# Kernel tuning notes

Measured on AMD Instinct MI355X. Metric: run time of the kernel, lower is better.

The kernel has to match this reference:

```python
import jax, jax.numpy as jnp
import numpy as np

H = 24  # hidden size hard-coded in TrendGRU


def setup_inputs() -> dict:
    key = jax.random.key(0)
    ks = jax.random.split(key, 7)
    B, T = 32768, 512
    s_ih = 1.0 / np.sqrt(H)
    x = jax.random.normal(ks[0], (B, T, 1), dtype=jnp.float32)
    # GRUCell params (PyTorch layout: rows ordered r, z, n)
    W_ih = jax.random.uniform(ks[1], (3 * H, 1), minval=-s_ih, maxval=s_ih, dtype=jnp.float32)
    W_hh = jax.random.uniform(ks[2], (3 * H, H), minval=-s_ih, maxval=s_ih, dtype=jnp.float32)
    b_ih = jax.random.uniform(ks[3], (3 * H,), minval=-s_ih, maxval=s_ih, dtype=jnp.float32)
    b_hh = jax.random.uniform(ks[4], (3 * H,), minval=-s_ih, maxval=s_ih, dtype=jnp.float32)
    fc_w = jax.random.uniform(ks[5], (2, H), minval=-s_ih, maxval=s_ih, dtype=jnp.float32)
    fc_b = jax.random.uniform(ks[6], (2,), minval=-s_ih, maxval=s_ih, dtype=jnp.float32)
    return {"x": x, "W_ih": W_ih, "b_ih": b_ih, "W_hh": W_hh, "b_hh": b_hh,
            "fc_w": fc_w, "fc_b": fc_b}


def _gru_scan(x, W_ih, b_ih, W_hh, b_hh):
    B = x.shape[0]
    # precompute input projections for all timesteps: (B,T,1)@(1,3H) -> (T,B,3H)
    gx = jnp.einsum('bti,gi->tbg', x, W_ih) + b_ih
    h0 = jnp.zeros((B, H), dtype=x.dtype)

    def step(h, gx_t):
        gh = h @ W_hh.T + b_hh                      # (B, 3H)
        xr, xz, xn = jnp.split(gx_t, 3, axis=-1)    # PyTorch order r, z, n
        hr, hz, hn = jnp.split(gh, 3, axis=-1)
        r = jax.nn.sigmoid(xr + hr)
        z = jax.nn.sigmoid(xz + hz)
        n = jnp.tanh(xn + r * hn)
        h_new = (1.0 - z) * n + z * h
        return h_new, None

    h_final, _ = jax.lax.scan(step, h0, gx)
    return h_final


def reference(x, W_ih, b_ih, W_hh, b_hh, fc_w, fc_b):
    h = _gru_scan(x, W_ih, b_ih, W_hh, b_hh)
    return h @ fc_w.T + fc_b  # (B, 2)
```

## Files before the change

### kernel.cpp

```cpp
#include <hip/hip_runtime.h>


#define GRU_T 512
#define FS 28

typedef __attribute__((ext_vector_type(8)))  short bf16x8;
typedef __attribute__((ext_vector_type(16))) float f32x16;
typedef __attribute__((ext_vector_type(2)))  float f32x2;
typedef __attribute__((ext_vector_type(2)))  unsigned uint2v;

__device__ __forceinline__ float bf16hi_f(float v) {
    unsigned u = __float_as_uint(v);
    u = (u + 0x7FFFu + ((u >> 16) & 1u)) & 0xFFFF0000u;
    return __uint_as_float(u);
}
__device__ __forceinline__ unsigned bf16_rne(float v) {
    unsigned u = __float_as_uint(v);
    return (u + 0x7FFFu + ((u >> 16) & 1u)) >> 16;
}
__device__ __forceinline__ unsigned cvt_pk_bf16(float lo, float hi) {
    unsigned r;
    asm("v_cvt_pk_bf16_f32 %0, %1, %2" : "=v"(r) : "v"(lo), "v"(hi));
    return r;
}
__device__ __forceinline__ f32x16 mfma32(bf16x8 a, bf16x8 b, f32x16 c) {
    return __builtin_amdgcn_mfma_f32_32x32x16_bf16(a, b, c, 0, 0, 0);
}

__global__ __launch_bounds__(64) void trend_gru_mfma32(
    const float* __restrict__ x,
    const float* __restrict__ W_ih,
    const float* __restrict__ b_ih,
    const float* __restrict__ W_hh,
    const float* __restrict__ b_hh,
    const float* __restrict__ fc_w,
    const float* __restrict__ fc_b,
    float* __restrict__ out)
{
    const int lane = threadIdx.x;
    const int e    = lane & 31;
    const int half = lane >> 5;
    const int elem0 = blockIdx.x * 32;

    __shared__ __align__(16) float Flds[32 * FS];

    const float L2E = 1.4426950408889634f;

    bf16x8 A[3][2][2];
#pragma unroll
    for (int g = 0; g < 3; ++g) {
        const float sc = (g == 2) ? 2.0f * L2E : L2E;
        const int m = e;
        const bool valid = m < 24;
        const int R = g * 24 + (valid ? m : 0);
        const float wx = (g < 2 && valid) ? sc * W_ih[R] : 0.0f;
        const float bb = valid ? sc * ((g < 2) ? (b_ih[R] + b_hh[R]) : b_hh[R]) : 0.0f;
        const float wxh = bf16hi_f(wx), bbh = bf16hi_f(bb);
#pragma unroll
        for (int s = 0; s < 2; ++s) {
            bf16x8 fh, fl;
#pragma unroll
            for (int jj = 0; jj < 8; ++jj) {
                const int k = s * 16 + half * 8 + jj;
                float vh = 0.0f, vl = 0.0f;
                if (valid && k < 24) {
                    const float w  = sc * W_hh[R * 24 + k];
                    const float wh = bf16hi_f(w);
                    vh = wh; vl = w - wh;
                } else if (valid) {
                    if (k == 24 || k == 25)      vh = wxh;
                    else if (k == 26)            vh = wx - wxh;
                    else if (k == 27)            vh = bbh;
                    else if (k == 28)            vh = bb - bbh;
                }
                fh[jj] = (short)bf16_rne(vh);
                fl[jj] = (short)bf16_rne(vl);
            }
            A[g][s][0] = fh;
            A[g][s][1] = fl;
        }
    }

    f32x2 wn2[6], bn2[6];
#pragma unroll
    for (int p = 0; p < 6; ++p) {
#pragma unroll
        for (int c = 0; c < 2; ++c) {
            const int s = p * 2 + c;
            const int j = (s & 3) + 8 * (s >> 2) + 4 * half;
            wn2[p][c] = 2.0f * L2E * W_ih[48 + j];
            bn2[p][c] = 2.0f * L2E * b_ih[48 + j];
        }
    }

    const float* xp = x + (size_t)(elem0 + e) * GRU_T;
    float xv = xp[0];

    f32x2 h2[6];
#pragma unroll
    for (int p = 0; p < 6; ++p) { h2[p].x = 0.0f; h2[p].y = 0.0f; }

    f32x2 aX2[6];
#pragma unroll
    for (int p = 0; p < 6; ++p) {
        const f32x2 xb = {xv, xv};
        aX2[p] = __builtin_elementwise_fma(wn2[p], xb, bn2[p]);
    }

    unsigned P0 = 0, P1 = 0, P2 = 0, P3 = 0, P4 = 0, P5 = 0;

    const f32x16 z16 = {0.f,0.f,0.f,0.f,0.f,0.f,0.f,0.f,
                        0.f,0.f,0.f,0.f,0.f,0.f,0.f,0.f};

#pragma unroll 2
    for (int t = 0; t < GRU_T; ++t) {
        const uint2v r02 = __builtin_amdgcn_permlane32_swap(P0, P2, false, false);
        const uint2v r13 = __builtin_amdgcn_permlane32_swap(P1, P3, false, false);
        uint4 b0q;
        b0q.x = r02.x;
        b0q.y = r13.x;
        b0q.z = r02.y;
        b0q.w = r13.y;

        const uint2v r44 = __builtin_amdgcn_permlane32_swap(P4, P4, false, false);
        const uint2v r55 = __builtin_amdgcn_permlane32_swap(P5, P5, false, false);
        uint4 b1q;
        b1q.x = P4;
        b1q.y = P5;
        b1q.z = r44.y;
        b1q.w = r55.y;
        if (half) {
            const unsigned xy = cvt_pk_bf16(xv, 1.0f);
            const float    xh = __uint_as_float(xy << 16);
            const unsigned xx = cvt_pk_bf16(xv, xv - xh);
            b1q.x = xx;
            b1q.y = xy;
            b1q.z = 0x00003F80u;
            b1q.w = 0u;
        }
        const bf16x8 B0 = *(const bf16x8*)&b0q;
        const bf16x8 B1 = *(const bf16x8*)&b1q;
        const float xnext = xp[(t + 1 < GRU_T) ? t + 1 : t];

        f32x16 aR = mfma32(A[0][0][0], B0, z16);
        aR = mfma32(A[0][0][1], B0, aR);
        aR = mfma32(A[0][1][0], B1, aR);
        aR = mfma32(A[0][1][1], B1, aR);
        f32x16 aZ = mfma32(A[1][0][0], B0, z16);
        aZ = mfma32(A[1][0][1], B0, aZ);
        aZ = mfma32(A[1][1][0], B1, aZ);
        aZ = mfma32(A[1][1][1], B1, aZ);
        f32x16 aN = mfma32(A[2][0][0], B0, z16);
        aN = mfma32(A[2][0][1], B0, aN);
        aN = mfma32(A[2][1][0], B1, aN);
        aN = mfma32(A[2][1][1], B1, aN);

#pragma unroll
        for (int G = 0; G < 3; ++G) {
            unsigned pk[2];
#pragma unroll
            for (int p = 0; p < 2; ++p) {
                const int s = G * 4 + p * 2;
                f32x2 er2, ez2, qi2, ev2, rv2;
                er2.x = __builtin_amdgcn_exp2f(-aR[s]);
                er2.y = __builtin_amdgcn_exp2f(-aR[s + 1]);
                ez2.x = __builtin_amdgcn_exp2f(-aZ[s]);
                ez2.y = __builtin_amdgcn_exp2f(-aZ[s + 1]);
                const f32x2 one2 = {1.0f, 1.0f};
                const f32x2 dr2 = er2 + one2;
                const f32x2 dz2 = ez2 + one2;
                const f32x2 pp2 = dr2 * dz2;
                qi2.x = __builtin_amdgcn_rcpf(pp2.x);
                qi2.y = __builtin_amdgcn_rcpf(pp2.y);
                const f32x2 rr2 = qi2 * dz2;
                const f32x2 zz2 = qi2 * dr2;
                const f32x2 an2 = {aN[s], aN[s + 1]};
                const f32x2 u2  = __builtin_elementwise_fma(rr2, an2, aX2[G * 2 + p]);
                ev2.x = __builtin_amdgcn_exp2f(u2.x);
                ev2.y = __builtin_amdgcn_exp2f(u2.y);
                const f32x2 dv2 = ev2 + one2;
                rv2.x = __builtin_amdgcn_rcpf(dv2.x);
                rv2.y = __builtin_amdgcn_rcpf(dv2.y);
                const f32x2 m2   = {-2.0f, -2.0f};
                const f32x2 nn2  = __builtin_elementwise_fma(m2, rv2, one2);
                const f32x2 hm2  = h2[G * 2 + p] - nn2;
                const f32x2 hn2  = __builtin_elementwise_fma(zz2, hm2, nn2);
                h2[G * 2 + p] = hn2;
                pk[p] = cvt_pk_bf16(hn2.x, hn2.y);
            }
            if (G == 0)      { P0 = pk[0]; P1 = pk[1]; }
            else if (G == 1) { P2 = pk[0]; P3 = pk[1]; }
            else             { P4 = pk[0]; P5 = pk[1]; }
        }

        xv = xnext;
#pragma unroll
        for (int p = 0; p < 6; ++p) {
            const f32x2 xb = {xv, xv};
            aX2[p] = __builtin_elementwise_fma(wn2[p], xb, bn2[p]);
        }
    }

#pragma unroll
    for (int G = 0; G < 3; ++G) {
        float4 f4;
        f4.x = h2[G * 2 + 0].x; f4.y = h2[G * 2 + 0].y;
        f4.z = h2[G * 2 + 1].x; f4.w = h2[G * 2 + 1].y;
        *(float4*)(&Flds[e * FS + G * 8 + half * 4]) = f4;
    }
    if (lane < 32) {
        float o0 = fc_b[0], o1 = fc_b[1];
#pragma unroll
        for (int j = 0; j < 24; ++j) {
            const float hv = Flds[lane * FS + j];
            o0 = fmaf(hv, fc_w[j],      o0);
            o1 = fmaf(hv, fc_w[24 + j], o1);
        }
        float2 o; o.x = o0; o.y = o1;
        *(float2*)(out + (size_t)(elem0 + lane) * 2) = o;
    }
}

extern "C" void kernel_launch(void* const* d_in, const int* in_sizes, int n_in,
                              void* d_out, int out_size, void* d_ws, size_t ws_size,
                              hipStream_t stream) {
    const float* x    = (const float*)d_in[0];
    const float* W_ih = (const float*)d_in[1];
    const float* b_ih = (const float*)d_in[2];
    const float* W_hh = (const float*)d_in[3];
    const float* b_hh = (const float*)d_in[4];
    const float* fc_w = (const float*)d_in[5];
    const float* fc_b = (const float*)d_in[6];
    float* out = (float*)d_out;

    const int B = in_sizes[0] / GRU_T;
    const int grid = B / 32;
    trend_gru_mfma32<<<grid, 64, 0, stream>>>(x, W_ih, b_ih, W_hh, b_hh,
                                              fc_w, fc_b, out);
}
```

Measured before the change: 454.5 us.

## Software-pipeline GRU step so B1 MFMAs overlap remaining gate epilogue

Restructures the recurrence loop so that the hidden-state slice feeding the second MFMA operand (P4/P5 plus the x/bias terms) is computed first. Its MFMAs are issued while the epilogue for the other four pairs is still running, and accumulation order is reversed so the B0 MFMAs finish the accumulator. Each pair also shares a single reciprocal between two lanes' denominators for both the sigmoid and tanh paths, cutting transcendental ops. The aim is to hide MFMA latency on the serial critical path, at the cost of extra live accumulator registers, a peeled prologue/epilogue, and a slight precision change from the shared reciprocal.

```diff
diff --git a/kernel.cpp b/kernel.cpp
--- a/kernel.cpp
+++ b/kernel.cpp
@@ -25,6 +25,39 @@
 }
 __device__ __forceinline__ f32x16 mfma32(bf16x8 a, bf16x8 b, f32x16 c) {
     return __builtin_amdgcn_mfma_f32_32x32x16_bf16(a, b, c, 0, 0, 0);
+}
+
+__device__ __forceinline__ unsigned pair_epi(float ar0, float ar1,
+                                             float az0, float az1,
+                                             float an0, float an1,
+                                             const f32x2 aX, f32x2& h)
+{
+    const f32x2 one2 = {1.0f, 1.0f};
+    f32x2 er2, ez2, ev2;
+    er2.x = __builtin_amdgcn_exp2f(-ar0);
+    er2.y = __builtin_amdgcn_exp2f(-ar1);
+    ez2.x = __builtin_amdgcn_exp2f(-az0);
+    ez2.y = __builtin_amdgcn_exp2f(-az1);
+    const f32x2 dr2 = er2 + one2;
+    const f32x2 dz2 = ez2 + one2;
+    const f32x2 pp2 = dr2 * dz2;
+    const float  Q  = __builtin_amdgcn_rcpf(pp2.x * pp2.y);
+    f32x2 qi2; qi2.x = Q * pp2.y; qi2.y = Q * pp2.x;
+    const f32x2 rr2 = qi2 * dz2;
+    const f32x2 zz2 = qi2 * dr2;
+    const f32x2 an2 = {an0, an1};
+    const f32x2 u2  = __builtin_elementwise_fma(rr2, an2, aX);
+    ev2.x = __builtin_amdgcn_exp2f(u2.x);
+    ev2.y = __builtin_amdgcn_exp2f(u2.y);
+    const f32x2 dv2 = ev2 + one2;
+    const float  Qn = __builtin_amdgcn_rcpf(dv2.x * dv2.y);
+    f32x2 rv2; rv2.x = Qn * dv2.y; rv2.y = Qn * dv2.x;
+    const f32x2 m2  = {-2.0f, -2.0f};
+    const f32x2 nn2 = __builtin_elementwise_fma(m2, rv2, one2);
+    const f32x2 hm2 = h - nn2;
+    const f32x2 hn2 = __builtin_elementwise_fma(zz2, hm2, nn2);
+    h = hn2;
+    return cvt_pk_bf16(hn2.x, hn2.y);
 }
 
 __global__ __launch_bounds__(64) void trend_gru_mfma32(
@@ -94,11 +127,16 @@
     }
 
     const float* xp = x + (size_t)(elem0 + e) * GRU_T;
-    float xv = xp[0];
 
     f32x2 h2[6];
 #pragma unroll
     for (int p = 0; p < 6; ++p) { h2[p].x = 0.0f; h2[p].y = 0.0f; }
+
+    const f32x16 z16 = {0.f,0.f,0.f,0.f,0.f,0.f,0.f,0.f,
+                        0.f,0.f,0.f,0.f,0.f,0.f,0.f,0.f};
+
+    float xv    = xp[0];
+    float xnext = xp[1];
 
     f32x2 aX2[6];
 #pragma unroll
@@ -107,99 +145,88 @@
         aX2[p] = __builtin_elementwise_fma(wn2[p], xb, bn2[p]);
     }
 
-    unsigned P0 = 0, P1 = 0, P2 = 0, P3 = 0, P4 = 0, P5 = 0;
-
-    const f32x16 z16 = {0.f,0.f,0.f,0.f,0.f,0.f,0.f,0.f,
-                        0.f,0.f,0.f,0.f,0.f,0.f,0.f,0.f};
-
-#pragma unroll 2
-    for (int t = 0; t < GRU_T; ++t) {
-        const uint2v r02 = __builtin_amdgcn_permlane32_swap(P0, P2, false, false);
-        const uint2v r13 = __builtin_amdgcn_permlane32_swap(P1, P3, false, false);
+    f32x16 aR, aZ, aN;
+    {
+        uint4 b1q; b1q.x = 0u; b1q.y = 0u; b1q.z = 0u; b1q.w = 0u;
+        if (half) {
+            const unsigned xy = cvt_pk_bf16(xv, 1.0f);
+            const float    xh = __uint_as_float(xy << 16);
+            const unsigned xx = cvt_pk_bf16(xv, xv - xh);
+            b1q.x = xx; b1q.y = xy; b1q.z = 0x00003F80u; b1q.w = 0u;
+        }
+        const bf16x8 B1 = *(const bf16x8*)&b1q;
+        uint4 b0q; b0q.x = 0u; b0q.y = 0u; b0q.z = 0u; b0q.w = 0u;
+        const bf16x8 B0 = *(const bf16x8*)&b0q;
+        aR = mfma32(A[0][1][0], B1, mfma32(A[0][1][1], B1, z16));
+        aZ = mfma32(A[1][1][0], B1, mfma32(A[1][1][1], B1, z16));
+        aN = mfma32(A[2][1][0], B1, mfma32(A[2][1][1], B1, z16));
+        aR = mfma32(A[0][0][0], B0, mfma32(A[0][0][1], B0, aR));
+        aZ = mfma32(A[1][0][0], B0, mfma32(A[1][0][1], B0, aZ));
+        aN = mfma32(A[2][0][0], B0, mfma32(A[2][0][1], B0, aN));
+    }
+
+#pragma unroll 1
+    for (int t = 0; t < GRU_T - 1; ++t) {
+        const unsigned nP4 = pair_epi(aR[8],  aR[9],  aZ[8],  aZ[9],
+                                      aN[8],  aN[9],  aX2[4], h2[4]);
+        const unsigned nP5 = pair_epi(aR[10], aR[11], aZ[10], aZ[11],
+                                      aN[10], aN[11], aX2[5], h2[5]);
+        const uint2v r44 = __builtin_amdgcn_permlane32_swap(nP4, nP4, false, false);
+        const uint2v r55 = __builtin_amdgcn_permlane32_swap(nP5, nP5, false, false);
+        uint4 b1q;
+        b1q.x = nP4;
+        b1q.y = nP5;
+        b1q.z = r44.y;
+        b1q.w = r55.y;
+        if (half) {
+            const unsigned xy = cvt_pk_bf16(xnext, 1.0f);
+            const float    xh = __uint_as_float(xy << 16);
+            const unsigned xx = cvt_pk_bf16(xnext, xnext - xh);
+            b1q.x = xx; b1q.y = xy; b1q.z = 0x00003F80u; b1q.w = 0u;
+        }
+        const bf16x8 B1 = *(const bf16x8*)&b1q;
+
+        f32x16 nR = mfma32(A[0][1][0], B1, mfma32(A[0][1][1], B1, z16));
+        f32x16 nZ = mfma32(A[1][1][0], B1, mfma32(A[1][1][1], B1, z16));
+        f32x16 nN = mfma32(A[2][1][0], B1, mfma32(A[2][1][1], B1, z16));
+
+        const unsigned nP0 = pair_epi(aR[0], aR[1], aZ[0], aZ[1],
+                                      aN[0], aN[1], aX2[0], h2[0]);
+        const unsigned nP1 = pair_epi(aR[2], aR[3], aZ[2], aZ[3],
+                                      aN[2], aN[3], aX2[1], h2[1]);
+        const unsigned nP2 = pair_epi(aR[4], aR[5], aZ[4], aZ[5],
+                                      aN[4], aN[5], aX2[2], h2[2]);
+        const unsigned nP3 = pair_epi(aR[6], aR[7], aZ[6], aZ[7],
+                                      aN[6], aN[7], aX2[3], h2[3]);
+        const uint2v r02 = __builtin_amdgcn_permlane32_swap(nP0, nP2, false, false);
+        const uint2v r13 = __builtin_amdgcn_permlane32_swap(nP1, nP3, false, false);
         uint4 b0q;
         b0q.x = r02.x;
         b0q.y = r13.x;
         b0q.z = r02.y;
         b0q.w = r13.y;
-
-        const uint2v r44 = __builtin_amdgcn_permlane32_swap(P4, P4, false, false);
-        const uint2v r55 = __builtin_amdgcn_permlane32_swap(P5, P5, false, false);
-        uint4 b1q;
-        b1q.x = P4;
-        b1q.y = P5;
-        b1q.z = r44.y;
-        b1q.w = r55.y;
-        if (half) {
-            const unsigned xy = cvt_pk_bf16(xv, 1.0f);
-            const float    xh = __uint_as_float(xy << 16);
-            const unsigned xx = cvt_pk_bf16(xv, xv - xh);
-            b1q.x = xx;
-            b1q.y = xy;
-            b1q.z = 0x00003F80u;
-            b1q.w = 0u;
-        }
         const bf16x8 B0 = *(const bf16x8*)&b0q;
-        const bf16x8 B1 = *(const bf16x8*)&b1q;
-        const float xnext = xp[(t + 1 < GRU_T) ? t + 1 : t];
-
-        f32x16 aR = mfma32(A[0][0][0], B0, z16);
-        aR = mfma32(A[0][0][1], B0, aR);
-        aR = mfma32(A[0][1][0], B1, aR);
-        aR = mfma32(A[0][1][1], B1, aR);
-        f32x16 aZ = mfma32(A[1][0][0], B0, z16);
-        aZ = mfma32(A[1][0][1], B0, aZ);
-        aZ = mfma32(A[1][1][0], B1, aZ);
-        aZ = mfma32(A[1][1][1], B1, aZ);
-        f32x16 aN = mfma32(A[2][0][0], B0, z16);
-        aN = mfma32(A[2][0][1], B0, aN);
-        aN = mfma32(A[2][1][0], B1, aN);
-        aN = mfma32(A[2][1][1], B1, aN);
-
-#pragma unroll
-        for (int G = 0; G < 3; ++G) {
-            unsigned pk[2];
-#pragma unroll
-            for (int p = 0; p < 2; ++p) {
-                const int s = G * 4 + p * 2;
-                f32x2 er2, ez2, qi2, ev2, rv2;
-                er2.x = __builtin_amdgcn_exp2f(-aR[s]);
-                er2.y = __builtin_amdgcn_exp2f(-aR[s + 1]);
-                ez2.x = __builtin_amdgcn_exp2f(-aZ[s]);
-                ez2.y = __builtin_amdgcn_exp2f(-aZ[s + 1]);
-                const f32x2 one2 = {1.0f, 1.0f};
-                const f32x2 dr2 = er2 + one2;
-                const f32x2 dz2 = ez2 + one2;
-                const f32x2 pp2 = dr2 * dz2;
-                qi2.x = __builtin_amdgcn_rcpf(pp2.x);
-                qi2.y = __builtin_amdgcn_rcpf(pp2.y);
-                const f32x2 rr2 = qi2 * dz2;
-                const f32x2 zz2 = qi2 * dr2;
-                const f32x2 an2 = {aN[s], aN[s + 1]};
-                const f32x2 u2  = __builtin_elementwise_fma(rr2, an2, aX2[G * 2 + p]);
-                ev2.x = __builtin_amdgcn_exp2f(u2.x);
-                ev2.y = __builtin_amdgcn_exp2f(u2.y);
-                const f32x2 dv2 = ev2 + one2;
-                rv2.x = __builtin_amdgcn_rcpf(dv2.x);
-                rv2.y = __builtin_amdgcn_rcpf(dv2.y);
-                const f32x2 m2   = {-2.0f, -2.0f};
-                const f32x2 nn2  = __builtin_elementwise_fma(m2, rv2, one2);
-                const f32x2 hm2  = h2[G * 2 + p] - nn2;
-                const f32x2 hn2  = __builtin_elementwise_fma(zz2, hm2, nn2);
-                h2[G * 2 + p] = hn2;
-                pk[p] = cvt_pk_bf16(hn2.x, hn2.y);
-            }
-            if (G == 0)      { P0 = pk[0]; P1 = pk[1]; }
-            else if (G == 1) { P2 = pk[0]; P3 = pk[1]; }
-            else             { P4 = pk[0]; P5 = pk[1]; }
-        }
-
-        xv = xnext;
+
+        nR = mfma32(A[0][0][0], B0, mfma32(A[0][0][1], B0, nR));
+        nZ = mfma32(A[1][0][0], B0, mfma32(A[1][0][1], B0, nZ));
+        nN = mfma32(A[2][0][0], B0, mfma32(A[2][0][1], B0, nN));
+
+        const float xcur = xnext;
+        xnext = xp[(t + 2 < GRU_T) ? t + 2 : GRU_T - 1];
 #pragma unroll
         for (int p = 0; p < 6; ++p) {
-            const f32x2 xb = {xv, xv};
+            const f32x2 xb = {xcur, xcur};
             aX2[p] = __builtin_elementwise_fma(wn2[p], xb, bn2[p]);
         }
-    }
+        aR = nR; aZ = nZ; aN = nN;
+    }
+
+    (void)pair_epi(aR[8],  aR[9],  aZ[8],  aZ[9],  aN[8],  aN[9],  aX2[4], h2[4]);
+    (void)pair_epi(aR[10], aR[11], aZ[10], aZ[11], aN[10], aN[11], aX2[5], h2[5]);
+    (void)pair_epi(aR[0],  aR[1],  aZ[0],  aZ[1],  aN[0],  aN[1],  aX2[0], h2[0]);
+    (void)pair_epi(aR[2],  aR[3],  aZ[2],  aZ[3],  aN[2],  aN[3],  aX2[1], h2[1]);
+    (void)pair_epi(aR[4],  aR[5],  aZ[4],  aZ[5],  aN[4],  aN[5],  aX2[2], h2[2]);
+    (void)pair_epi(aR[6],  aR[7],  aZ[6],  aZ[7],  aN[6],  aN[7],  aX2[3], h2[3]);
 
 #pragma unroll
     for (int G = 0; G < 3; ++G) {
@@ -208,6 +235,7 @@
         f4.z = h2[G * 2 + 1].x; f4.w = h2[G * 2 + 1].y;
         *(float4*)(&Flds[e * FS + G * 8 + half * 4]) = f4;
     }
+    __builtin_amdgcn_s_barrier();
     if (lane < 32) {
         float o0 = fc_b[0], o1 = fc_b[1];
 #pragma unroll
```

New measurement: 454.0 us. About the same (-0.1%).

## Replace transcendental exp2/rcp with packed polynomial exp2 and batched reciprocals

Applied to the files above, without the earlier changes.

Swaps the hardware exp2 (transcendental unit) for a packed-FMA polynomial exp2 built on exponent bit manipulation, so the work can use packed VALU instead of the quarter-rate transcendental pipe. It also shares one rcp across four values using the product trick (Montgomery-style batched inversion), cutting rcp count fourfold. x loads are changed to float4 per four timesteps, prefetching the next group. The costs are more VALU instructions, a risk of overflow or underflow in the batched product and in the exponent shift for large inputs, and a small change in accuracy.

```diff
diff --git a/kernel.cpp b/kernel.cpp
--- a/kernel.cpp
+++ b/kernel.cpp
@@ -25,6 +25,80 @@
 }
 __device__ __forceinline__ f32x16 mfma32(bf16x8 a, bf16x8 b, f32x16 c) {
     return __builtin_amdgcn_mfma_f32_32x32x16_bf16(a, b, c, 0, 0, 0);
+}
+
+__device__ __forceinline__ f32x2 exp2_core(f32x2 zf, f32x2 z) {
+    const f32x2 C5 = {1.3333558e-3f, 1.3333558e-3f};
+    const f32x2 C4 = {9.6181291e-3f, 9.6181291e-3f};
+    const f32x2 C3 = {5.5504109e-2f, 5.5504109e-2f};
+    const f32x2 C2 = {2.4022651e-1f, 2.4022651e-1f};
+    const f32x2 C1 = {6.9314718e-1f, 6.9314718e-1f};
+    const f32x2 one2 = {1.0f, 1.0f};
+    f32x2 p = __builtin_elementwise_fma(C5, zf, C4);
+    p = __builtin_elementwise_fma(p, zf, C3);
+    p = __builtin_elementwise_fma(p, zf, C2);
+    p = __builtin_elementwise_fma(p, zf, C1);
+    p = __builtin_elementwise_fma(p, zf, one2);
+    const unsigned r0 = __float_as_uint(p.x) + (__float_as_uint(z.x) << 23);
+    const unsigned r1 = __float_as_uint(p.y) + (__float_as_uint(z.y) << 23);
+    f32x2 o; o.x = __uint_as_float(r0); o.y = __uint_as_float(r1);
+    return o;
+}
+__device__ __forceinline__ f32x2 exp2p_pk(f32x2 x) {
+    const f32x2 MAG = {0x1.8p23f, 0x1.8p23f};
+    const f32x2 z  = x + MAG;
+    const f32x2 n2 = z - MAG;
+    const f32x2 zf = x - n2;
+    return exp2_core(zf, z);
+}
+__device__ __forceinline__ f32x2 exp2n_pk(f32x2 x) {
+    const f32x2 MAG = {0x1.8p23f, 0x1.8p23f};
+    const f32x2 z  = MAG - x;
+    const f32x2 n2 = z - MAG;
+    const f32x2 s  = x + n2;
+    const f32x2 zf = -s;
+    return exp2_core(zf, z);
+}
+
+__device__ __forceinline__ void g_epi(const f32x2 ar0, const f32x2 ar1,
+                                      const f32x2 az0, const f32x2 az1,
+                                      const f32x2 an0, const f32x2 an1,
+                                      const f32x2 aX0, const f32x2 aX1,
+                                      f32x2& h0, f32x2& h1,
+                                      unsigned& o0, unsigned& o1)
+{
+    const f32x2 one2 = {1.0f, 1.0f};
+    const f32x2 er0 = exp2n_pk(ar0), er1 = exp2n_pk(ar1);
+    const f32x2 ez0 = exp2n_pk(az0), ez1 = exp2n_pk(az1);
+    const f32x2 dr0 = er0 + one2, dr1 = er1 + one2;
+    const f32x2 dz0 = ez0 + one2, dz1 = ez1 + one2;
+    const f32x2 pp0 = dr0 * dz0, pp1 = dr1 * dz1;
+    const float  s0 = pp0.x * pp0.y, s1 = pp1.x * pp1.y;
+    const float  QS = __builtin_amdgcn_rcpf(s0 * s1);
+    const float  Q0 = QS * s1, Q1 = QS * s0;
+    f32x2 qi0, qi1;
+    qi0.x = Q0 * pp0.y; qi0.y = Q0 * pp0.x;
+    qi1.x = Q1 * pp1.y; qi1.y = Q1 * pp1.x;
+    const f32x2 rr0 = qi0 * dz0, rr1 = qi1 * dz1;
+    const f32x2 zz0 = qi0 * dr0, zz1 = qi1 * dr1;
+    const f32x2 u0 = __builtin_elementwise_fma(rr0, an0, aX0);
+    const f32x2 u1 = __builtin_elementwise_fma(rr1, an1, aX1);
+    const f32x2 ev0 = exp2p_pk(u0), ev1 = exp2p_pk(u1);
+    const f32x2 dv0 = ev0 + one2, dv1 = ev1 + one2;
+    const float  t0 = dv0.x * dv0.y, t1 = dv1.x * dv1.y;
+    const float  QT = __builtin_amdgcn_rcpf(t0 * t1);
+    const float  T0 = QT * t1, T1 = QT * t0;
+    f32x2 rv0, rv1;
+    rv0.x = T0 * dv0.y; rv0.y = T0 * dv0.x;
+    rv1.x = T1 * dv1.y; rv1.y = T1 * dv1.x;
+    const f32x2 m2 = {-2.0f, -2.0f};
+    const f32x2 nn0 = __builtin_elementwise_fma(m2, rv0, one2);
+    const f32x2 nn1 = __builtin_elementwise_fma(m2, rv1, one2);
+    const f32x2 hn0 = __builtin_elementwise_fma(zz0, h0 - nn0, nn0);
+    const f32x2 hn1 = __builtin_elementwise_fma(zz1, h1 - nn1, nn1);
+    h0 = hn0; h1 = hn1;
+    o0 = cvt_pk_bf16(hn0.x, hn0.y);
+    o1 = cvt_pk_bf16(hn1.x, hn1.y);
 }
 
 __global__ __launch_bounds__(64) void trend_gru_mfma32(
@@ -94,111 +168,89 @@
     }
 
     const float* xp = x + (size_t)(elem0 + e) * GRU_T;
-    float xv = xp[0];
 
     f32x2 h2[6];
 #pragma unroll
     for (int p = 0; p < 6; ++p) { h2[p].x = 0.0f; h2[p].y = 0.0f; }
-
-    f32x2 aX2[6];
-#pragma unroll
-    for (int p = 0; p < 6; ++p) {
-        const f32x2 xb = {xv, xv};
-        aX2[p] = __builtin_elementwise_fma(wn2[p], xb, bn2[p]);
-    }
 
     unsigned P0 = 0, P1 = 0, P2 = 0, P3 = 0, P4 = 0, P5 = 0;
 
     const f32x16 z16 = {0.f,0.f,0.f,0.f,0.f,0.f,0.f,0.f,
                         0.f,0.f,0.f,0.f,0.f,0.f,0.f,0.f};
 
-#pragma unroll 2
-    for (int t = 0; t < GRU_T; ++t) {
-        const uint2v r02 = __builtin_amdgcn_permlane32_swap(P0, P2, false, false);
-        const uint2v r13 = __builtin_amdgcn_permlane32_swap(P1, P3, false, false);
-        uint4 b0q;
-        b0q.x = r02.x;
-        b0q.y = r13.x;
-        b0q.z = r02.y;
-        b0q.w = r13.y;
-
-        const uint2v r44 = __builtin_amdgcn_permlane32_swap(P4, P4, false, false);
-        const uint2v r55 = __builtin_amdgcn_permlane32_swap(P5, P5, false, false);
-        uint4 b1q;
-        b1q.x = P4;
-        b1q.y = P5;
-        b1q.z = r44.y;
-        b1q.w = r55.y;
-        if (half) {
+    float4 xq = *(const float4*)(xp);
+#pragma unroll 1
+    for (int t4 = 0; t4 < GRU_T / 4; ++t4) {
+        const int nxt = (t4 < GRU_T / 4 - 1) ? (t4 * 4 + 4) : (GRU_T - 4);
+        const float4 xqn = *(const float4*)(xp + nxt);
+#pragma unroll
+        for (int tt = 0; tt < 4; ++tt) {
+            const float xv = (tt == 0) ? xq.x : (tt == 1) ? xq.y
+                           : (tt == 2) ? xq.z : xq.w;
+
             const unsigned xy = cvt_pk_bf16(xv, 1.0f);
             const float    xh = __uint_as_float(xy << 16);
             const unsigned xx = cvt_pk_bf16(xv, xv - xh);
-            b1q.x = xx;
-            b1q.y = xy;
-            b1q.z = 0x00003F80u;
-            b1q.w = 0u;
-        }
-        const bf16x8 B0 = *(const bf16x8*)&b0q;
-        const bf16x8 B1 = *(const bf16x8*)&b1q;
-        const float xnext = xp[(t + 1 < GRU_T) ? t + 1 : t];
-
-        f32x16 aR = mfma32(A[0][0][0], B0, z16);
-        aR = mfma32(A[0][0][1], B0, aR);
-        aR = mfma32(A[0][1][0], B1, aR);
-        aR = mfma32(A[0][1][1], B1, aR);
-        f32x16 aZ = mfma32(A[1][0][0], B0, z16);
-        aZ = mfma32(A[1][0][1], B0, aZ);
-        aZ = mfma32(A[1][1][0], B1, aZ);
-        aZ = mfma32(A[1][1][1], B1, aZ);
-        f32x16 aN = mfma32(A[2][0][0], B0, z16);
-        aN = mfma32(A[2][0][1], B0, aN);
-        aN = mfma32(A[2][1][0], B1, aN);
-        aN = mfma32(A[2][1][1], B1, aN);
-
-#pragma unroll
-        for (int G = 0; G < 3; ++G) {
-            unsigned pk[2];
-#pragma unroll
-            for (int p = 0; p < 2; ++p) {
-                const int s = G * 4 + p * 2;
-                f32x2 er2, ez2, qi2, ev2, rv2;
-                er2.x = __builtin_amdgcn_exp2f(-aR[s]);
-                er2.y = __builtin_amdgcn_exp2f(-aR[s + 1]);
-                ez2.x = __builtin_amdgcn_exp2f(-aZ[s]);
-                ez2.y = __builtin_amdgcn_exp2f(-aZ[s + 1]);
-                const f32x2 one2 = {1.0f, 1.0f};
-                const f32x2 dr2 = er2 + one2;
-                const f32x2 dz2 = ez2 + one2;
-                const f32x2 pp2 = dr2 * dz2;
-                qi2.x = __builtin_amdgcn_rcpf(pp2.x);
-                qi2.y = __builtin_amdgcn_rcpf(pp2.y);
-                const f32x2 rr2 = qi2 * dz2;
-                const f32x2 zz2 = qi2 * dr2;
-                const f32x2 an2 = {aN[s], aN[s + 1]};
-                const f32x2 u2  = __builtin_elementwise_fma(rr2, an2, aX2[G * 2 + p]);
-                ev2.x = __builtin_amdgcn_exp2f(u2.x);
-                ev2.y = __builtin_amdgcn_exp2f(u2.y);
-                const f32x2 dv2 = ev2 + one2;
-                rv2.x = __builtin_amdgcn_rcpf(dv2.x);
-                rv2.y = __builtin_amdgcn_rcpf(dv2.y);
-                const f32x2 m2   = {-2.0f, -2.0f};
-                const f32x2 nn2  = __builtin_elementwise_fma(m2, rv2, one2);
-                const f32x2 hm2  = h2[G * 2 + p] - nn2;
-                const f32x2 hn2  = __builtin_elementwise_fma(zz2, hm2, nn2);
-                h2[G * 2 + p] = hn2;
-                pk[p] = cvt_pk_bf16(hn2.x, hn2.y);
-            }
-            if (G == 0)      { P0 = pk[0]; P1 = pk[1]; }
-            else if (G == 1) { P2 = pk[0]; P3 = pk[1]; }
-            else             { P4 = pk[0]; P5 = pk[1]; }
-        }
-
-        xv = xnext;
-#pragma unroll
-        for (int p = 0; p < 6; ++p) {
-            const f32x2 xb = {xv, xv};
-            aX2[p] = __builtin_elementwise_fma(wn2[p], xb, bn2[p]);
-        }
+            f32x2 aX2[6];
+#pragma unroll
+            for (int p = 0; p < 6; ++p) {
+                const f32x2 xb = {xv, xv};
+                aX2[p] = __builtin_elementwise_fma(wn2[p], xb, bn2[p]);
+            }
+
+            const uint2v r02 = __builtin_amdgcn_permlane32_swap(P0, P2, false, false);
+            const uint2v r13 = __builtin_amdgcn_permlane32_swap(P1, P3, false, false);
+            uint4 b0q;
+            b0q.x = r02.x;
+            b0q.y = r13.x;
+            b0q.z = r02.y;
+            b0q.w = r13.y;
+
+            const uint2v r44 = __builtin_amdgcn_permlane32_swap(P4, P4, false, false);
+            const uint2v r55 = __builtin_amdgcn_permlane32_swap(P5, P5, false, false);
+            uint4 b1q;
+            b1q.x = P4;
+            b1q.y = P5;
+            b1q.z = r44.y;
+            b1q.w = r55.y;
+            if (half) {
+                b1q.x = xx; b1q.y = xy; b1q.z = 0x00003F80u; b1q.w = 0u;
+            }
+            const bf16x8 B0 = *(const bf16x8*)&b0q;
+            const bf16x8 B1 = *(const bf16x8*)&b1q;
+
+            f32x16 aR = mfma32(A[0][0][0], B0, z16);
+            aR = mfma32(A[0][0][1], B0, aR);
+            aR = mfma32(A[0][1][0], B1, aR);
+            aR = mfma32(A[0][1][1], B1, aR);
+            f32x16 aZ = mfma32(A[1][0][0], B0, z16);
+            aZ = mfma32(A[1][0][1], B0, aZ);
+            aZ = mfma32(A[1][1][0], B1, aZ);
+            aZ = mfma32(A[1][1][1], B1, aZ);
+            f32x16 aN = mfma32(A[2][0][0], B0, z16);
+            aN = mfma32(A[2][0][1], B0, aN);
+            aN = mfma32(A[2][1][0], B1, aN);
+            aN = mfma32(A[2][1][1], B1, aN);
+
+#pragma unroll
+            for (int G = 0; G < 3; ++G) {
+                f32x2 ar0, ar1, az0, az1, an0, an1;
+                ar0.x = aR[G * 4 + 0]; ar0.y = aR[G * 4 + 1];
+                ar1.x = aR[G * 4 + 2]; ar1.y = aR[G * 4 + 3];
+                az0.x = aZ[G * 4 + 0]; az0.y = aZ[G * 4 + 1];
+                az1.x = aZ[G * 4 + 2]; az1.y = aZ[G * 4 + 3];
+                an0.x = aN[G * 4 + 0]; an0.y = aN[G * 4 + 1];
+                an1.x = aN[G * 4 + 2]; an1.y = aN[G * 4 + 3];
+                unsigned pa, pb;
+                g_epi(ar0, ar1, az0, az1, an0, an1,
+                      aX2[G * 2], aX2[G * 2 + 1],
+                      h2[G * 2], h2[G * 2 + 1], pa, pb);
+                if (G == 0)      { P0 = pa; P1 = pb; }
+                else if (G == 1) { P2 = pa; P3 = pb; }
+                else             { P4 = pa; P5 = pb; }
+            }
+        }
+        xq = xqn;
     }
 
 #pragma unroll
```

Result: slower. 541.1 us (+19.0%).
